# Kernel tuning notes

Measured on AMD Instinct MI355X. Metric: run time of the kernel, lower is better.

The kernel has to match this reference:

```python
import jax, jax.numpy as jnp
import numpy as np

B_IN, B_MID, B_OUT = 30, 16, 10   # band widths: input sphere, after S2 conv, after SO3 conv
F1, F2 = 100, 100                 # feature channels
EPS = 1e-5


def _qw(b):
    """Driscoll-Healy quadrature weights over the 2b beta samples (SOFT grid)."""
    j = np.arange(2 * b)
    k = np.arange(b)
    s = (np.sin(np.pi * (2 * j[:, None] + 1) * (2 * k[None, :] + 1) / (4 * b))
         / (2 * k[None, :] + 1)).sum(1)
    return ((2.0 / b) * np.sin(np.pi * (2 * j + 1) / (4 * b)) * s).astype(np.float32)


def _wigner_d_all(l_max, betas):
    """Wigner-d matrices d^l(beta) = exp(-i beta Jy) in the |l,m> basis (m = -l..l).
    Returns list over l of real arrays [n_beta, 2l+1, 2l+1]."""
    betas = np.asarray(betas, np.float64)
    out = []
    for l in range(l_max):
        m = np.arange(-l, l + 1)
        dim = 2 * l + 1
        Jp = np.zeros((dim, dim))
        for i in range(dim - 1):
            Jp[i + 1, i] = np.sqrt(l * (l + 1) - m[i] * (m[i] + 1))
        Jy = (Jp - Jp.T) / 2j
        ev, V = np.linalg.eigh(Jy)
        ph = np.exp(-1j * betas[:, None] * ev[None, :])
        d = np.einsum('ak,bk,ck->bac', V, ph, V.conj())
        out.append(np.real(d).astype(np.float32))
    return out


def _project(x, b):
    """Radial max-projection of a point cloud [B,3,N] onto a (beta,alpha) grid -> [B,1,2b,2b]."""
    r = jnp.sqrt(jnp.sum(x * x, axis=1) + 1e-12)                       # [B,N]
    beta = jnp.arccos(jnp.clip(x[:, 2] / r, -1 + 1e-7, 1 - 1e-7))      # [0,pi]
    alpha = jnp.mod(jnp.arctan2(x[:, 1], x[:, 0]), 2 * np.pi)          # [0,2pi)
    jb = jnp.clip((beta / np.pi * (2 * b)).astype(jnp.int32), 0, 2 * b - 1)
    ja = jnp.clip((alpha / (2 * np.pi) * (2 * b)).astype(jnp.int32), 0, 2 * b - 1)
    flat = jb * (2 * b) + ja
    img = jax.vmap(lambda f, v: jnp.zeros((2 * b) ** 2, x.dtype).at[f].max(v))(flat, r)
    return img.reshape(x.shape[0], 1, 2 * b, 2 * b)


def _s2_fft(x, dm0_w):
    """x: [B,F,2b,2b] (beta,alpha) -> list over l of x_hat [B,F,2l+1] (complex)."""
    X = jnp.fft.fft(x, axis=-1)     # FFT over alpha
    n = x.shape[-1]
    hats = []
    for l, dw in enumerate(dm0_w):
        idx = np.mod(np.arange(-l, l + 1), n)
        hats.append(jnp.einsum('pm,BFpm->BFm', jnp.asarray(dw), X[..., idx]))
    return hats


def _so3_fft(x, dmn_w):
    """x: [B,F,2b,2b,2b] (beta,alpha,gamma) -> list over l of [B,F,2l+1,2l+1]."""
    X = jnp.fft.fftn(x, axes=(-2, -1))   # FFT over alpha, gamma
    n = x.shape[-1]
    hats = []
    for l, dw in enumerate(dmn_w):
        idx = np.mod(np.arange(-l, l + 1), n)
        Xl = X[:, :, :, idx[:, None], idx[None, :]]        # [B,F,2b,2l+1,2l+1]
        hats.append(jnp.einsum('pmn,BFpmn->BFmn', jnp.asarray(dw), Xl))
    return hats


def _so3_ifft(hats, b, d_list):
    """list over l of [B,F,2l+1,2l+1] -> real SO(3) signal [B,F,2b,2b,2b]."""
    Bb, Ff = hats[0].shape[:2]
    n = 2 * b
    Fg = jnp.zeros((Bb, Ff, n, n, n), jnp.complex64)   # (beta, m, n) freq grid
    for l, h in enumerate(hats):
        idx = np.mod(np.arange(-l, l + 1), n)
        c = (2 * l + 1) * jnp.einsum('pmn,BFmn->BFpmn', jnp.asarray(d_list[l]), h)
        Fg = Fg.at[:, :, :, idx[:, None], idx[None, :]].add(c)
    return jnp.real(jnp.fft.ifft2(Fg, axes=(-2, -1)))


def _bn_relu(x, g, b):
    mu = jnp.mean(x, axis=(0, 2, 3, 4), keepdims=True)
    var = jnp.var(x, axis=(0, 2, 3, 4), keepdims=True)
    xn = (x - mu) * jax.lax.rsqrt(var + EPS)
    return jax.nn.relu(xn * g[None, :, None, None, None] + b[None, :, None, None, None])


def _forward(x, w_s2, b_s2, bn1_gamma, bn1_beta, w_so3, b_so3, bn2_gamma, bn2_beta):
    # constant tables (numpy, computed eagerly)
    betas_in = (np.arange(2 * B_IN) + 0.5) * np.pi / (2 * B_IN)
    betas_mid = (np.arange(2 * B_MID) + 0.5) * np.pi / (2 * B_MID)
    betas_out = (np.arange(2 * B_OUT) + 0.5) * np.pi / (2 * B_OUT)
    w_in, w_mid, w_out = _qw(B_IN), _qw(B_MID), _qw(B_OUT)
    d_in = _wigner_d_all(B_MID, betas_in)
    d_mid = _wigner_d_all(B_MID, betas_mid)
    d_out = _wigner_d_all(B_OUT, betas_out)
    d_eq = _wigner_d_all(B_MID, np.array([np.pi / 2]))   # equatorial grid beta = pi/2

    img = _project(x, B_IN)                              # [B,1,60,60]

    # ---- S2 convolution: band 30 -> 16 ----
    dm0_w = [d_in[l][:, :, l] * w_in[:, None] for l in range(B_MID)]   # d^l_{m0} * quad weights
    xhat = _s2_fft(img, dm0_w)                           # list of [B,1,2l+1]
    k_s2 = w_s2.shape[-1]
    a_s2 = 2 * np.pi * np.arange(k_s2) / k_s2
    ws = w_s2 * np.float32(1.0 / np.sqrt(k_s2 * 1 * B_MID ** 4 / B_IN ** 2))
    zhat = []
    for l in range(B_MID):
        m = np.arange(-l, l + 1)
        sh = (d_eq[l][0][:, l][None, :] * np.exp(-1j * np.outer(a_s2, m))).astype(np.complex64)  # [k,m]
        yh = jnp.einsum('km,iok->mio', jnp.asarray(sh), ws)           # kernel spectrum [2l+1,f_in,f_out]
        zhat.append(jnp.einsum('Bim,nio->Bomn', xhat[l], jnp.conj(yh)))  # outer product m x n
    z = _so3_ifft(zhat, B_MID, d_mid) + b_s2[None, :, None, None, None]  # [B,100,32,32,32]
    z = _bn_relu(z, bn1_gamma, bn1_beta)

    # ---- SO3 convolution: band 16 -> 10 ----
    dmn_w = [d_mid[l] * w_mid[:, None, None] for l in range(B_OUT)]
    xhat2 = _so3_fft(z, dmn_w)                           # list of [B,100,2l+1,2l+1]
    k_so3 = w_so3.shape[-1]
    a_so3 = 2 * np.pi * np.arange(k_so3) / k_so3
    wk = w_so3 * np.float32(1.0 / np.sqrt(k_so3 * F1 * B_OUT ** 3 / B_MID ** 3))
    zhat2 = []
    for l in range(B_OUT):
        m = np.arange(-l, l + 1)
        U = (d_eq[l][0][None] * np.exp(-1j * np.outer(a_so3, m))[:, :, None]).astype(np.complex64)  # [k,m,n], gamma=0
        yh = jnp.einsum('kmn,iok->mnio', jnp.asarray(U), wk)
        zhat2.append(jnp.einsum('Bimk,nkio->Bomn', xhat2[l], jnp.conj(yh)))  # z^l = x^l y^l+
    z2 = _so3_ifft(zhat2, B_OUT, d_out) + b_so3[None, :, None, None, None]   # [B,100,20,20,20]
    z2 = _bn_relu(z2, bn2_gamma, bn2_beta)

    # ---- so3_integrate: sum over alpha/gamma, quadrature-weighted sum over beta ----
    return jnp.einsum('BCpag,p->BC', z2, jnp.asarray(w_out))   # [B,100]


def setup_inputs() -> dict:
    key = jax.random.key(0)
    k0, k1, k2 = jax.random.split(key, 3)
    B, N = 8, 2048
    return {
        "x": jax.random.normal(k0, (B, 3, N), jnp.float32),
        "w_s2": jax.random.normal(k1, (1, F1, 2 * B_IN), jnp.float32),
        "b_s2": jnp.zeros((F1,), jnp.float32),
        "bn1_gamma": jnp.ones((F1,), jnp.float32),
        "bn1_beta": jnp.zeros((F1,), jnp.float32),
        "w_so3": jax.random.normal(k2, (F1, F2, 2 * B_MID), jnp.float32),
        "b_so3": jnp.zeros((F2,), jnp.float32),
        "bn2_gamma": jnp.ones((F2,), jnp.float32),
        "bn2_beta": jnp.zeros((F2,), jnp.float32),
    }


def reference(x, w_s2, b_s2, bn1_gamma, bn1_beta, w_so3, b_so3, bn2_gamma, bn2_beta):
    return _forward(x, w_s2, b_s2, bn1_gamma, bn1_beta, w_so3, b_so3, bn2_gamma, bn2_beta)
```

## Files before the change

### kernel.cpp

```cpp
#include <hip/hip_runtime.h>
#include <math.h>

#define PI_D 3.14159265358979323846

constexpr int NBATCH = 8;
constexpr int NPTS   = 2048;
constexpr int F1C    = 100;
constexpr int F2C    = 100;

__host__ __device__ constexpr int S2c(int l){ return l*(2*l-1)*(2*l+1)/3; }

constexpr int OFF_WIN   = 0;
constexpr int OFF_WMID  = OFF_WIN + 60;
constexpr int OFF_WOUTQ = OFF_WMID + 32;
constexpr int OFF_DM0W  = OFF_WOUTQ + 20;
constexpr int OFF_DMID  = OFF_DM0W + 60*256;
constexpr int OFF_DOUT  = OFF_DMID + 32*S2c(16);
constexpr int OFF_DEQ   = OFF_DOUT + 20*S2c(10);
constexpr int OFF_IMG   = OFF_DEQ + S2c(16);
constexpr int OFF_XF    = OFF_IMG + NBATCH*60*60;
constexpr int OFF_XHAT  = OFF_XF + NBATCH*60*31*2;
constexpr int OFF_WS2   = OFF_XHAT + NBATCH*256*2;
constexpr int OFF_BN1   = OFF_WS2 + 100*31*2;
constexpr int OFF_BN1AB = OFF_BN1 + 200;
constexpr int OFF_BN2   = OFF_BN1AB + 200;
constexpr int OFF_BN2AB = OFF_BN2 + 200;
constexpr int OFF_LUTA  = OFF_BN2AB + 200;
constexpr int OFF_LUTB  = OFF_LUTA + 1330;
constexpr int OFF_WCONV = OFF_LUTB + 1330;
constexpr int OFF_XHAT2 = OFF_WCONV + 100*100*19*2;
constexpr int OFF_SBUF  = OFF_XHAT2 + NBATCH*100*S2c(10)*2;
constexpr int OFF_ZHAT2 = OFF_SBUF + NBATCH*100*S2c(10)*2;
constexpr int OFF_Z2    = OFF_ZHAT2 + NBATCH*100*S2c(10)*2;
constexpr int OFF_Z     = OFF_Z2 + NBATCH*100*20*20*20;
constexpr int WS_TOTAL  = OFF_Z + NBATCH*100*32*32*32;
constexpr int OFF_HBUF  = OFF_Z2;

__device__ __forceinline__ int S2d(int l){ return l*(2*l-1)*(2*l+1)/3; }

__global__ void k_quad(float* ws){
  int j = threadIdx.x;
  if (j < 60){
    double bb = 30.0, s = 0.0;
    for (int k = 0; k < 30; ++k) s += sin(PI_D*(2*j+1)*(2*k+1)/(4.0*bb))/(2*k+1);
    ws[OFF_WIN+j] = (float)(2.0/bb * sin(PI_D*(2*j+1)/(4.0*bb)) * s);
  }
  if (j < 32){
    double bb = 16.0, s = 0.0;
    for (int k = 0; k < 16; ++k) s += sin(PI_D*(2*j+1)*(2*k+1)/(4.0*bb))/(2*k+1);
    ws[OFF_WMID+j] = (float)(2.0/bb * sin(PI_D*(2*j+1)/(4.0*bb)) * s);
  }
  if (j < 20){
    double bb = 10.0, s = 0.0;
    for (int k = 0; k < 10; ++k) s += sin(PI_D*(2*j+1)*(2*k+1)/(4.0*bb))/(2*k+1);
    ws[OFF_WOUTQ+j] = (float)(2.0/bb * sin(PI_D*(2*j+1)/(4.0*bb)) * s);
  }
}

__global__ void k_lut(float* ws){
  int q = blockIdx.x*blockDim.x + threadIdx.x;
  if (q >= 1330) return;
  int l = 0; while (S2d(l+1) <= q) ++l;
  int loc = q - S2d(l), tl = 2*l+1;
  int mm = loc/tl, nn = loc%tl;
  ((int*)(ws+OFF_LUTA))[q] = 32*S2d(l) + mm*tl + nn;
  ((int*)(ws+OFF_LUTB))[q] = ((mm-l+9)*19 + (nn-l+9)) | ((tl*tl) << 9) | ((nn-l+9) << 19);
}

__device__ double dev_wigner_t(const double* fact, int l, int mp, int m, double beta){
  double ch = cos(0.5*beta), sh = sin(0.5*beta);
  int kmin = m - mp; if (kmin < 0) kmin = 0;
  int kmax = l + m; if (l - mp < kmax) kmax = l - mp;
  double pref = sqrt(fact[l+mp]*fact[l-mp]*fact[l+m]*fact[l-m]);
  int ec = 2*l + m - mp - 2*kmin, es = mp - m + 2*kmin;
  double cp = 1.0, sp = 1.0;
  for (int e = 0; e < ec; ++e) cp *= ch;
  for (int e = 0; e < es; ++e) sp *= sh;
  double ch2i = 1.0/(ch*ch), sh2 = sh*sh;
  double sum = 0.0;
  for (int k = kmin; k <= kmax; ++k){
    double t = 1.0/(fact[l+m-k]*fact[k]*fact[l-mp-k]*fact[mp-m+k]);
    if ((mp-m+k) & 1) t = -t;
    sum += t*cp*sp;
    cp *= ch2i; sp *= sh2;
  }
  return pref*sum;
}

constexpr int N_DM0W = 60*256;
constexpr int N_DMID = 32*S2c(16);
constexpr int N_DOUT = 20*S2c(10);
constexpr int N_DEQ  = S2c(16);
constexpr int N_WIG  = N_DM0W + N_DMID + N_DOUT + N_DEQ;

__global__ void k_wigner(float* ws){
  __shared__ double fact[32];
  if (threadIdx.x == 0){ fact[0] = 1.0; for (int i = 1; i < 32; ++i) fact[i] = fact[i-1]*i; }
  __syncthreads();
  int idx = blockIdx.x*blockDim.x + threadIdx.x;
  if (idx >= N_WIG) return;
  if (idx < N_DM0W){
    int l = 0; while (60*(l+1)*(l+1) <= idx) ++l;
    int rem = idx - 60*l*l, tl = 2*l+1;
    int p = rem/tl, mm = rem%tl;
    double beta = (p+0.5)*PI_D/60.0;
    ws[OFF_DM0W+idx] = (float)dev_wigner_t(fact, l, mm-l, 0, beta) * ws[OFF_WIN+p];
    return;
  }
  idx -= N_DM0W;
  if (idx < N_DMID){
    int l = 0; while (32*S2d(l+1) <= idx) ++l;
    int rem = idx - 32*S2d(l), tl = 2*l+1;
    int q = rem % (tl*tl), p = rem/(tl*tl);
    int mm = q/tl, nn = q%tl;
    double beta = (p+0.5)*PI_D/32.0;
    ws[OFF_DMID+idx] = (float)dev_wigner_t(fact, l, mm-l, nn-l, beta);
    return;
  }
  idx -= N_DMID;
  if (idx < N_DOUT){
    int l = 0; while (20*S2d(l+1) <= idx) ++l;
    int rem = idx - 20*S2d(l), tl = 2*l+1;
    int q = rem % (tl*tl), p = rem/(tl*tl);
    int mm = q/tl, nn = q%tl;
    double beta = (p+0.5)*PI_D/20.0;
    ws[OFF_DOUT+idx] = (float)dev_wigner_t(fact, l, mm-l, nn-l, beta);
    return;
  }
  idx -= N_DOUT;
  {
    int l = 0; while (S2d(l+1) <= idx) ++l;
    int rem = idx - S2d(l), tl = 2*l+1;
    int mm = rem/tl, nn = rem%tl;
    ws[OFF_DEQ+idx] = (float)dev_wigner_t(fact, l, mm-l, nn-l, 0.5*PI_D);
  }
}

__global__ void k_project(const float* __restrict__ x, float* ws){
  int t = blockIdx.x*blockDim.x + threadIdx.x;
  if (t >= NBATCH*NPTS) return;
  int b = t / NPTS, n = t % NPTS;
  const float* xb = x + (size_t)b*3*NPTS;
  float xx = xb[n], yy = xb[NPTS+n], zz = xb[2*NPTS+n];
  float r = sqrtf(xx*xx + yy*yy + zz*zz + 1e-12f);
  float ct = zz / r;
  ct = fminf(fmaxf(ct, -1.0f + 1e-7f), 1.0f - 1e-7f);
  float beta = acosf(ct);
  float alpha = atan2f(yy, xx);
  if (alpha < 0.0f) alpha += 2.0f*(float)PI_D;
  int jb = (int)((beta / (float)PI_D) * 60.0f);
  jb = jb < 0 ? 0 : (jb > 59 ? 59 : jb);
  int ja = (int)((alpha / (2.0f*(float)PI_D)) * 60.0f);
  ja = ja < 0 ? 0 : (ja > 59 ? 59 : ja);
  unsigned* img = (unsigned*)(ws + OFF_IMG) + (b*3600 + jb*60 + ja);
  atomicMax(img, __float_as_uint(r));
}

__global__ void k_s2dft(float* ws){
  int t = blockIdx.x*blockDim.x + threadIdx.x;
  if (t >= NBATCH*60*31) return;
  int b = t/(60*31), r = t%(60*31);
  int p = r/31, mi = r%31, m = mi - 15;
  const float* img = ws + OFF_IMG + (b*60 + p)*60;
  float sr = 0.f, si = 0.f;
  for (int a = 0; a < 60; ++a){
    int k = ((a*m) % 60 + 60) % 60;
    float c = cospif(k/30.0f), s = sinpif(k/30.0f);
    float v = img[a];
    sr += v*c; si -= v*s;
  }
  ws[OFF_XF + t*2]   = sr;
  ws[OFF_XF + t*2+1] = si;
}

__global__ void k_xhat(float* ws){
  int t = blockIdx.x*blockDim.x + threadIdx.x;
  if (t >= NBATCH*256) return;
  int b = t/256, flat = t%256;
  int l = 0; while ((l+1)*(l+1) <= flat) ++l;
  int mm = flat - l*l, tl = 2*l+1;
  int mi = mm - l + 15;
  float sr = 0.f, si = 0.f;
  for (int p = 0; p < 60; ++p){
    float w = ws[OFF_DM0W + 60*l*l + p*tl + mm];
    sr += w * ws[OFF_XF + ((b*60+p)*31 + mi)*2];
    si += w * ws[OFF_XF + ((b*60+p)*31 + mi)*2 + 1];
  }
  ws[OFF_XHAT + t*2]   = sr;
  ws[OFF_XHAT + t*2+1] = si;
}

__global__ void k_ws2(float* ws, const float* __restrict__ w_s2, float scale1){
  int t = blockIdx.x*blockDim.x + threadIdx.x;
  if (t >= 100*31) return;
  int o = t/31, ni = t%31, n = ni - 15;
  float sr = 0.f, si = 0.f;
  for (int k = 0; k < 60; ++k){
    int kk = ((k*n) % 60 + 60) % 60;
    float c = cospif(kk/30.0f), s = sinpif(kk/30.0f);
    float v = w_s2[o*60 + k] * scale1;
    sr += v*c; si += v*s;
  }
  ws[OFF_WS2 + t*2]   = sr;
  ws[OFF_WS2 + t*2+1] = si;
}

__global__ __launch_bounds__(256) void k_H(float* ws){
  int bid = blockIdx.x;
  int p = bid & 31, b = bid >> 5;
  __shared__ float xh[512], Dt[256];
  __shared__ int dbase[16];
  int tid = threadIdx.x;
  {
    int flat = tid;
    int l = 0; while ((l+1)*(l+1) <= flat) ++l;
    int mm = flat - l*l, tl = 2*l+1;
    xh[2*flat]   = ws[OFF_XHAT + (b*256+flat)*2];
    xh[2*flat+1] = ws[OFF_XHAT + (b*256+flat)*2+1];
    Dt[flat] = (float)tl * ws[OFF_DEQ + S2d(l) + mm*tl + l];
  }
  if (tid < 16){ int l = tid, tl = 2*l+1; dbase[l] = OFF_DMID + 32*S2d(l) + p*tl*tl; }
  __syncthreads();
  float* Hb = ws + OFF_HBUF + (size_t)bid*992;
  for (int q = tid; q < 496; q += 256){
    int m = q/31, ni = q%31, n = ni-15;
    int an = n < 0 ? -n : n;
    int lmin = m > an ? m : an;
    float ar = 0.f, ai = 0.f;
    for (int l = lmin; l < 16; ++l){
      int tl = 2*l+1;
      float d = ws[dbase[l] + (m+l)*tl + (n+l)];
      float t = d * Dt[l*l + (n+l)];
      int fa = l*l + (m+l);
      ar += t*xh[2*fa]; ai += t*xh[2*fa+1];
    }
    Hb[2*q] = ar; Hb[2*q+1] = ai;
  }
}

__global__ __launch_bounds__(256) void k_so3ifft_mid(float* ws, const float* __restrict__ b_s2){
  int bid = blockIdx.x;
  int p = bid & 31, bo = bid >> 5;
  int o = bo % F1C, b = bo / F1C;
  __shared__ float Fg[992], tmpS[1024];
  __shared__ float twr[32], twi[32], Wr[31], Wi[31], redA[4], redB[4];
  int tid = threadIdx.x;
  if (tid < 32){ twr[tid] = cospif(tid/16.0f); twi[tid] = sinpif(tid/16.0f); }
  if (tid < 31){ Wr[tid] = ws[OFF_WS2 + (o*31+tid)*2]; Wi[tid] = ws[OFF_WS2 + (o*31+tid)*2+1]; }
  __syncthreads();
  {
    const float* Hb = ws + OFF_HBUF + (size_t)((b<<5)|p)*992;
    for (int q = tid; q < 496; q += 256){
      int ni = q % 31;
      float hr = Hb[2*q], hi = Hb[2*q+1];
      float wr = Wr[ni], wi = Wi[ni];
      Fg[2*q]   = hr*wr - hi*wi;
      Fg[2*q+1] = hr*wi + hi*wr;
    }
  }
  __syncthreads();
  if (tid < 128){
    int m = tid >> 3, g0 = tid & 7;
    float T0r=0,T0i=0,T1r=0,T1i=0,T2r=0,T2i=0,T3r=0,T3i=0;
    int base = 2*m*31;
    #pragma unroll
    for (int ni = 0; ni < 31; ++ni){
      int k = ((ni-15)*g0) & 31;
      float c = twr[k], s = twi[k];
      float fr = Fg[base+2*ni], fi = Fg[base+2*ni+1];
      float re = fr*c - fi*s, im = fr*s + fi*c;
      int cc = (ni+1) & 3;
      if (cc == 0){ T0r += re; T0i += im; }
      else if (cc == 1){ T1r += re; T1i += im; }
      else if (cc == 2){ T2r += re; T2i += im; }
      else { T3r += re; T3i += im; }
    }
    float Ar=T0r+T2r, Ai=T0i+T2i, Br=T0r-T2r, Bi=T0i-T2i;
    float Cr=T1r+T3r, Ci=T1i+T3i, Dr=T1r-T3r, Di=T1i-T3i;
    int ix = 2*(m*32+g0);
    tmpS[ix]      = Ar+Cr; tmpS[ix+1]    = Ai+Ci;
    tmpS[ix+16]   = Br-Di; tmpS[ix+17]   = Bi+Dr;
    tmpS[ix+32]   = Ar-Cr; tmpS[ix+33]   = Ai-Ci;
    tmpS[ix+48]   = Br+Di; tmpS[ix+49]   = Bi-Dr;
  }
  __syncthreads();
  float bsv = b_s2[o];
  float lsum = 0.f, lss = 0.f;
  float* z = ws + OFF_Z;
  size_t zb = ((size_t)(b*F1C+o)*32 + p)*1024;
  {
    int a0 = tid >> 5, g = tid & 31;
    float U0r=0, U2r=0, U1r=0, U1i=0, U3r=0, U3i=0;
    #pragma unroll
    for (int m = 1; m < 16; ++m){
      int k = (m*a0) & 31;
      float c = twr[k], s = twi[k];
      float tr = tmpS[2*(m*32+g)], ti = tmpS[2*(m*32+g)+1];
      float re = tr*c - ti*s;
      int cc = m & 3;
      if (cc == 0) U0r += re;
      else if (cc == 2) U2r += re;
      else {
        float im = tr*s + ti*c;
        if (cc == 1){ U1r += re; U1i += im; }
        else        { U3r += re; U3i += im; }
      }
    }
    float Ar = U0r + U2r, Br = U0r - U2r;
    float Cr = U1r + U3r, Di = U1i - U3i;
    float t0 = tmpS[2*g];
    float v0 = (t0 + 2.0f*(Ar + Cr))*(1.0f/1024.0f) + bsv;
    float v1 = (t0 + 2.0f*(Br - Di))*(1.0f/1024.0f) + bsv;
    float v2 = (t0 + 2.0f*(Ar - Cr))*(1.0f/1024.0f) + bsv;
    float v3 = (t0 + 2.0f*(Br + Di))*(1.0f/1024.0f) + bsv;
    z[zb + (a0     )*32 + g] = v0;
    z[zb + (a0 +  8)*32 + g] = v1;
    z[zb + (a0 + 16)*32 + g] = v2;
    z[zb + (a0 + 24)*32 + g] = v3;
    lsum = v0+v1+v2+v3;
    lss  = v0*v0+v1*v1+v2*v2+v3*v3;
  }
  for (int off = 32; off; off >>= 1){ lsum += __shfl_down(lsum, off); lss += __shfl_down(lss, off); }
  if ((tid & 63) == 0){ redA[tid>>6] = lsum; redB[tid>>6] = lss; }
  __syncthreads();
  if (tid == 0){
    atomicAdd(&ws[OFF_BN1 + o],       redA[0]+redA[1]+redA[2]+redA[3]);
    atomicAdd(&ws[OFF_BN1 + 100 + o], redB[0]+redB[1]+redB[2]+redB[3]);
  }
}

__global__ void k_bnfin1(float* ws, const float* __restrict__ g1, const float* __restrict__ be1){
  int t = threadIdx.x;
  if (t >= 100) return;
  const float invN = 1.0f/262144.0f;
  float mu = ws[OFF_BN1+t]*invN;
  float var = ws[OFF_BN1+100+t]*invN - mu*mu;
  float sA = rsqrtf(var + 1e-5f) * g1[t];
  ws[OFF_BN1AB+t]     = sA;
  ws[OFF_BN1AB+100+t] = be1[t] - mu*sA;
}

__global__ __launch_bounds__(256) void k_so3fft_a(float* ws){
  int bid = blockIdx.x;
  int p = bid & 31, bo = bid >> 5;
  int o = bo % F1C;
  __shared__ float y[32*33];
  __shared__ float Bs[32*36];
  __shared__ float t1[1216];
  __shared__ float twr[32], twi[32];
  int tid = threadIdx.x;
  if (tid < 32){ twr[tid] = cospif(tid/16.0f); twi[tid] = sinpif(tid/16.0f); }
  float sA = ws[OFF_BN1AB+o], sB = ws[OFF_BN1AB+100+o];
  float* zp = ws + OFF_Z + (size_t)bid*1024;
  for (int q = tid; q < 1024; q += 256){
    float v = zp[q]*sA + sB;
    y[(q>>5)*33 + (q&31)] = v > 0.f ? v : 0.f;
  }
  __syncthreads();
  {
    int a = tid >> 3, g2 = tid & 7;
    float y0 = y[a*33+g2], y1 = y[a*33+g2+8], y2 = y[a*33+g2+16], y3 = y[a*33+g2+24];
    float e = y0+y2, f = y1+y3;
    int bb = a*36 + g2*4;
    Bs[bb]   = e+f;
    Bs[bb+1] = e-f;
    Bs[bb+2] = y0-y2;
    Bs[bb+3] = -(y1-y3);
  }
  __syncthreads();
  for (int q = tid; q < 320; q += 256){
    int a = q/10, n = q%10, ni = 9+n;
    int c = n & 3;
    int bb = a*36;
    float sr = 0.f, si = 0.f;
    if ((c & 1) == 0){
      int off = bb + (c >> 1);
      #pragma unroll
      for (int g2 = 0; g2 < 8; ++g2){
        int k = (g2*n) & 31;
        float B = Bs[off + g2*4];
        sr += B*twr[k]; si -= B*twi[k];
      }
    } else {
      float sgn = (c == 1) ? 1.f : -1.f;
      #pragma unroll
      for (int g2 = 0; g2 < 8; ++g2){
        int k = (g2*n) & 31;
        float cc_ = twr[k], ss = twi[k];
        float br = Bs[bb+g2*4+2], bi = sgn*Bs[bb+g2*4+3];
        sr += br*cc_ + bi*ss;
        si += bi*cc_ - br*ss;
      }
    }
    t1[2*(a*19+ni)] = sr; t1[2*(a*19+ni)+1] = si;
  }
  __syncthreads();
  for (int q = tid; q < 160; q += 256){
    int a = q/10, ni = 9 + q%10;
    int i0 = 2*(a*19+ni), i1 = 2*((a+16)*19+ni);
    float xr=t1[i0], xi=t1[i0+1], yr=t1[i1], yi=t1[i1+1];
    t1[i0]=xr+yr; t1[i0+1]=xi+yi; t1[i1]=xr-yr; t1[i1+1]=xi-yi;
  }
  __syncthreads();
  float wm = ws[OFF_WMID+p];
  for (int q = tid; q < 190; q += 256){
    int m = q/10 - 9, nio = q%10, ni = 9+nio;
    int off = (m & 1) ? 16*19 : 0;
    float sr = 0.f, si = 0.f;
    for (int a = 0; a < 16; ++a){
      int k = (a*m) & 31;
      float c = twr[k], s = twi[k];
      float tr = t1[2*(off+a*19+ni)], ti = t1[2*(off+a*19+ni)+1];
      sr += tr*c + ti*s;
      si += ti*c - tr*s;
    }
    sr *= wm; si *= wm;
    int qf = (m+9)*19 + ni;
    zp[2*qf] = sr; zp[2*qf+1] = si;
    if (nio > 0){
      int qm = (9-m)*19 + (9-nio);
      zp[2*qm] = sr; zp[2*qm+1] = -si;
    }
  }
}

__global__ __launch_bounds__(512) void k_so3fft_b(float* ws){
  int bo = blockIdx.x;
  int tid = threadIdx.x;
  __shared__ float xw[722];
  const float* xwbase = ws + OFF_Z + (size_t)bo*32*1024;
  const int* lutA = (const int*)(ws + OFF_LUTA);
  const int* lutB = (const int*)(ws + OFF_LUTB);
  float accr[3], acci[3];
  int la[3], xi2[3], tl2v[3];
  #pragma unroll
  for (int j = 0; j < 3; ++j){
    accr[j] = 0.f; acci[j] = 0.f;
    int q = tid + 512*j;
    if (q < 1330){ la[j] = lutA[q]; int lb = lutB[q]; xi2[j] = 2*(lb & 511); tl2v[j] = (lb >> 9) & 1023; }
    else { la[j] = 0; xi2[j] = 0; tl2v[j] = 0; }
  }
  for (int pp = 0; pp < 32; ++pp){
    __syncthreads();
    for (int u = tid; u < 722; u += 512) xw[u] = xwbase[pp*1024 + u];
    __syncthreads();
    #pragma unroll
    for (int j = 0; j < 3; ++j){
      int q = tid + 512*j;
      if (q < 1330){
        float d = ws[OFF_DMID + la[j] + pp*tl2v[j]];
        accr[j] += d*xw[xi2[j]]; acci[j] += d*xw[xi2[j]+1];
      }
    }
  }
  #pragma unroll
  for (int j = 0; j < 3; ++j){
    int q = tid + 512*j;
    if (q < 1330){
      int base = OFF_XHAT2 + (bo*1330 + q)*2;
      ws[base]   = accr[j];
      ws[base+1] = acci[j];
    }
  }
}

__global__ void k_wconv(float* ws, const float* __restrict__ w_so3, float scale2){
  int t = blockIdx.x*blockDim.x + threadIdx.x;
  if (t >= 100*100*19) return;
  int ni = t % 19, io = t / 19;
  int n = ni - 9;
  float sr = 0.f, si = 0.f;
  for (int j = 0; j < 32; ++j){
    int k = (j*n) & 31;
    float c = cospif(k/16.0f), s = sinpif(k/16.0f);
    float v = w_so3[io*32 + j] * scale2;
    sr += v*c; si += v*s;
  }
  ws[OFF_WCONV + t*2]   = sr;
  ws[OFF_WCONV + t*2+1] = si;
}

__global__ void k_S(float* ws){
  int t = blockIdx.x*blockDim.x + threadIdx.x;
  if (t >= NBATCH*100*1330) return;
  int q = t % 1330, bi = t / 1330;
  int l = 0; while (S2d(l+1) <= q) ++l;
  int loc = q - S2d(l), tl = 2*l+1;
  int mm = loc/tl, nn = loc%tl;
  float sr = 0.f, si = 0.f;
  int xbase = OFF_XHAT2 + (bi*1330 + S2d(l) + mm*tl)*2;
  int dbase = OFF_DEQ + S2d(l) + nn*tl;
  for (int k = 0; k < tl; ++k){
    float d = ws[dbase + k];
    sr += d * ws[xbase + 2*k];
    si += d * ws[xbase + 2*k + 1];
  }
  ws[OFF_SBUF + t*2]   = sr;
  ws[OFF_SBUF + t*2+1] = si;
}

__global__ void k_zhat2(float* ws){
  int t = blockIdx.x*blockDim.x + threadIdx.x;
  if (t >= NBATCH*100*1330) return;
  int q = t % 1330, bo = t / 1330;
  int o = bo % 100, b = bo / 100;
  int lb = ((const int*)(ws+OFF_LUTB))[q];
  int ni = (lb >> 19) & 31;
  const float* sp = ws + OFF_SBUF + (size_t)(b*100)*2660 + 2*q;
  const float* wp = ws + OFF_WCONV + (size_t)(o*19 + ni)*2;
  float sr = 0.f, si = 0.f;
  for (int i = 0; i < 100; ++i){
    float Sr = sp[0], Si = sp[1];
    float Wr = wp[0], Wi = wp[1];
    sr += Sr*Wr - Si*Wi;
    si += Sr*Wi + Si*Wr;
    sp += 2660;
    wp += 3800;
  }
  ws[OFF_ZHAT2 + ((size_t)bo*1330 + q)*2]     = sr;
  ws[OFF_ZHAT2 + ((size_t)bo*1330 + q)*2 + 1] = si;
}

__global__ __launch_bounds__(256) void k_so3ifft_out(float* ws, const float* __restrict__ b_so3){
  int bid = blockIdx.x;
  int pg = bid % 5, bo = bid / 5;
  int o = bo % F2C, b = bo / F2C;
  __shared__ __align__(16) float zh[2660];
  __shared__ float Fg[380], tmpS[400];
  __shared__ float twr[20], twi[20], redA[4], redB[4];
  int tid = threadIdx.x;
  {
    const float4* zsrc = (const float4*)(ws + OFF_ZHAT2 + (size_t)bo*2660);
    float4* zds = (float4*)zh;
    for (int q = tid; q < 665; q += 256) zds[q] = zsrc[q];
  }
  if (tid < 20){ twr[tid] = cospif(tid/10.0f); twi[tid] = sinpif(tid/10.0f); }
  __syncthreads();
  float bsv = b_so3[o];
  float lsum = 0.f, lss = 0.f;
  float* z2 = ws + OFF_Z2;
  for (int pp = 0; pp < 4; ++pp){
    int p = pg*4 + pp;
    for (int q = tid; q < 190; q += 256){
      int m = q/19, ni = q%19, n = ni-9;
      int an = n < 0 ? -n : n;
      int lmin = m > an ? m : an;
      float ar = 0.f, ai = 0.f;
      for (int l = lmin; l < 10; ++l){
        int tl = 2*l+1;
        float d = ws[OFF_DOUT + 20*S2d(l) + (p*tl + (m+l))*tl + (n+l)] * (float)tl;
        int fz = S2d(l) + (m+l)*tl + (n+l);
        ar += d*zh[2*fz]; ai += d*zh[2*fz+1];
      }
      Fg[2*q] = ar; Fg[2*q+1] = ai;
    }
    __syncthreads();
    for (int q = tid; q < 100; q += 256){
      int m = q/10, g = q%10;
      float Er=0.f, Ei=0.f, Or=0.f, Oi=0.f;
      int base = 2*m*19;
      for (int ni = 1; ni < 19; ni += 2){
        int n = ni-9;
        int k = ((n*g) % 20 + 20) % 20;
        float c = twr[k], s = twi[k];
        float fr = Fg[base+2*ni], fi = Fg[base+2*ni+1];
        Er += fr*c - fi*s; Ei += fr*s + fi*c;
      }
      for (int ni = 0; ni < 19; ni += 2){
        int n = ni-9;
        int k = ((n*g) % 20 + 20) % 20;
        float c = twr[k], s = twi[k];
        float fr = Fg[base+2*ni], fi = Fg[base+2*ni+1];
        Or += fr*c - fi*s; Oi += fr*s + fi*c;
      }
      tmpS[2*(m*20+g)]      = Er+Or; tmpS[2*(m*20+g)+1]      = Ei+Oi;
      tmpS[2*(m*20+g+10)]   = Er-Or; tmpS[2*(m*20+g+10)+1]   = Ei-Oi;
    }
    __syncthreads();
    size_t zb = ((size_t)bo*20 + p)*400;
    for (int q = tid; q < 200; q += 256){
      int a = q/20, g = q%20;
      float E = 0.f, O = 0.f;
      for (int m = 2; m < 10; m += 2){
        int k = (m*a) % 20;
        E += tmpS[2*(m*20+g)]*twr[k] - tmpS[2*(m*20+g)+1]*twi[k];
      }
      for (int m = 1; m < 10; m += 2){
        int k = (m*a) % 20;
        O += tmpS[2*(m*20+g)]*twr[k] - tmpS[2*(m*20+g)+1]*twi[k];
      }
      float t0 = tmpS[2*g];
      float v1 = (t0 + 2.0f*(E+O))*(1.0f/400.0f) + bsv;
      float v2 = (t0 + 2.0f*(E-O))*(1.0f/400.0f) + bsv;
      z2[zb + a*20 + g]       = v1;
      z2[zb + (a+10)*20 + g]  = v2;
      lsum += v1+v2; lss += v1*v1+v2*v2;
    }
    __syncthreads();
  }
  for (int off = 32; off; off >>= 1){ lsum += __shfl_down(lsum, off); lss += __shfl_down(lss, off); }
  if ((tid & 63) == 0){ redA[tid>>6] = lsum; redB[tid>>6] = lss; }
  __syncthreads();
  if (tid == 0){
    atomicAdd(&ws[OFF_BN2 + o],       redA[0]+redA[1]+redA[2]+redA[3]);
    atomicAdd(&ws[OFF_BN2 + 100 + o], redB[0]+redB[1]+redB[2]+redB[3]);
  }
}

__global__ void k_bnfin2(float* ws, const float* __restrict__ g2, const float* __restrict__ be2){
  int t = threadIdx.x;
  if (t >= 100) return;
  const float invN = 1.0f/64000.0f;
  float mu = ws[OFF_BN2+t]*invN;
  float var = ws[OFF_BN2+100+t]*invN - mu*mu;
  float sA = rsqrtf(var + 1e-5f) * g2[t];
  ws[OFF_BN2AB+t]     = sA;
  ws[OFF_BN2AB+100+t] = be2[t] - mu*sA;
}

__global__ __launch_bounds__(256) void k_final(float* ws, float* __restrict__ out){
  int bid = blockIdx.x;
  int c = bid % 100, b = bid / 100;
  int tid = threadIdx.x;
  float sA = ws[OFF_BN2AB+c], sB = ws[OFF_BN2AB+100+c];
  const float* z2 = ws + OFF_Z2 + (size_t)(b*100+c)*8000;
  float lsum = 0.f;
  for (int q = tid; q < 8000; q += 256){
    int p = q / 400;
    float v = z2[q]*sA + sB;
    v = v > 0.f ? v : 0.f;
    lsum += v * ws[OFF_WOUTQ + p];
  }
  for (int off = 32; off; off >>= 1) lsum += __shfl_down(lsum, off);
  __shared__ float red[4];
  if ((tid & 63) == 0) red[tid>>6] = lsum;
  __syncthreads();
  if (tid == 0) out[b*100 + c] = red[0]+red[1]+red[2]+red[3];
}

extern "C" void kernel_launch(void* const* d_in, const int* in_sizes, int n_in,
                              void* d_out, int out_size, void* d_ws, size_t ws_size,
                              hipStream_t stream){
  const float* x      = (const float*)d_in[0];
  const float* w_s2   = (const float*)d_in[1];
  const float* b_s2   = (const float*)d_in[2];
  const float* g1     = (const float*)d_in[3];
  const float* be1    = (const float*)d_in[4];
  const float* w_so3  = (const float*)d_in[5];
  const float* b_so3  = (const float*)d_in[6];
  const float* g2     = (const float*)d_in[7];
  const float* be2    = (const float*)d_in[8];
  float* ws  = (float*)d_ws;
  float* out = (float*)d_out;

  hipMemsetAsync(ws + OFF_IMG, 0, NBATCH*3600*sizeof(float), stream);
  hipMemsetAsync(ws + OFF_BN1, 0, 200*sizeof(float), stream);
  hipMemsetAsync(ws + OFF_BN2, 0, 200*sizeof(float), stream);

  k_quad<<<1, 128, 0, stream>>>(ws);
  k_lut<<<6, 256, 0, stream>>>(ws);
  k_wigner<<<(N_WIG + 255)/256, 256, 0, stream>>>(ws);
  k_project<<<(NBATCH*NPTS + 255)/256, 256, 0, stream>>>(x, ws);
  k_s2dft<<<(NBATCH*60*31 + 255)/256, 256, 0, stream>>>(ws);
  k_xhat<<<(NBATCH*256 + 255)/256, 256, 0, stream>>>(ws);
  float scale1 = (float)(1.0/sqrt(60.0*1.0*65536.0/900.0));
  k_ws2<<<(100*31 + 255)/256, 256, 0, stream>>>(ws, w_s2, scale1);
  k_H<<<NBATCH*32, 256, 0, stream>>>(ws);
  k_so3ifft_mid<<<NBATCH*F1C*32, 256, 0, stream>>>(ws, b_s2);
  k_bnfin1<<<1, 128, 0, stream>>>(ws, g1, be1);
  k_so3fft_a<<<NBATCH*F1C*32, 256, 0, stream>>>(ws);
  k_so3fft_b<<<NBATCH*F1C, 512, 0, stream>>>(ws);
  float scale2 = (float)(1.0/sqrt(32.0*100.0*1000.0/4096.0));
  k_wconv<<<(100*100*19 + 255)/256, 256, 0, stream>>>(ws, w_so3, scale2);
  k_S<<<(NBATCH*100*1330 + 255)/256, 256, 0, stream>>>(ws);
  k_zhat2<<<(NBATCH*100*1330 + 255)/256, 256, 0, stream>>>(ws);
  k_so3ifft_out<<<NBATCH*F2C*5, 256, 0, stream>>>(ws, b_so3);
  k_bnfin2<<<1, 128, 0, stream>>>(ws, g2, be2);
  k_final<<<NBATCH*100, 256, 0, stream>>>(ws, out);
}
```

Before: 541.2 us.

## Fuse S contraction into so3fft_b and process two channels per so3ifft_mid block

```diff
diff --git a/kernel.cpp b/kernel.cpp
--- a/kernel.cpp
+++ b/kernel.cpp
@@ -27,7 +27,8 @@
 constexpr int OFF_BN2AB = OFF_BN2 + 200;
 constexpr int OFF_LUTA  = OFF_BN2AB + 200;
 constexpr int OFF_LUTB  = OFF_LUTA + 1330;
-constexpr int OFF_WCONV = OFF_LUTB + 1330;
+constexpr int OFF_LUTC  = OFF_LUTB + 1330;
+constexpr int OFF_WCONV = OFF_LUTC + 1330;
 constexpr int OFF_XHAT2 = OFF_WCONV + 100*100*19*2;
 constexpr int OFF_SBUF  = OFF_XHAT2 + NBATCH*100*S2c(10)*2;
 constexpr int OFF_ZHAT2 = OFF_SBUF + NBATCH*100*S2c(10)*2;
@@ -65,6 +66,7 @@
   int mm = loc/tl, nn = loc%tl;
   ((int*)(ws+OFF_LUTA))[q] = 32*S2d(l) + mm*tl + nn;
   ((int*)(ws+OFF_LUTB))[q] = ((mm-l+9)*19 + (nn-l+9)) | ((tl*tl) << 9) | ((nn-l+9) << 19);
+  ((int*)(ws+OFF_LUTC))[q] = (S2d(l) + mm*tl) | ((S2d(l) + nn*tl) << 11) | (tl << 22);
 }
 
 __device__ double dev_wigner_t(const double* fact, int l, int mp, int m, double beta){
@@ -240,29 +242,37 @@
 
 __global__ __launch_bounds__(256) void k_so3ifft_mid(float* ws, const float* __restrict__ b_s2){
   int bid = blockIdx.x;
-  int p = bid & 31, bo = bid >> 5;
-  int o = bo % F1C, b = bo / F1C;
-  __shared__ float Fg[992], tmpS[1024];
-  __shared__ float twr[32], twi[32], Wr[31], Wi[31], redA[4], redB[4];
+  int p = bid & 31, boo = bid >> 5;
+  int oo = boo % 50, b = boo / 50;
+  int o0 = oo*2;
+  __shared__ float Fg[1984], tmpS[2048];
+  __shared__ float twr[32], twi[32], Wr[62], Wi[62], redA[8], redB[8];
   int tid = threadIdx.x;
   if (tid < 32){ twr[tid] = cospif(tid/16.0f); twi[tid] = sinpif(tid/16.0f); }
-  if (tid < 31){ Wr[tid] = ws[OFF_WS2 + (o*31+tid)*2]; Wi[tid] = ws[OFF_WS2 + (o*31+tid)*2+1]; }
+  if (tid < 62){
+    int oh = tid/31, ni = tid%31;
+    Wr[tid] = ws[OFF_WS2 + ((o0+oh)*31+ni)*2];
+    Wi[tid] = ws[OFF_WS2 + ((o0+oh)*31+ni)*2+1];
+  }
   __syncthreads();
   {
     const float* Hb = ws + OFF_HBUF + (size_t)((b<<5)|p)*992;
-    for (int q = tid; q < 496; q += 256){
-      int ni = q % 31;
-      float hr = Hb[2*q], hi = Hb[2*q+1];
-      float wr = Wr[ni], wi = Wi[ni];
+    for (int q = tid; q < 992; q += 256){
+      int half = q >= 496 ? 1 : 0;
+      int qq = q - half*496;
+      int ni = qq % 31;
+      float hr = Hb[2*qq], hi = Hb[2*qq+1];
+      float wr = Wr[half*31+ni], wi = Wi[half*31+ni];
       Fg[2*q]   = hr*wr - hi*wi;
       Fg[2*q+1] = hr*wi + hi*wr;
     }
   }
   __syncthreads();
-  if (tid < 128){
-    int m = tid >> 3, g0 = tid & 7;
+  {
+    int half = tid >> 7, w = tid & 127;
+    int m = w >> 3, g0 = w & 7;
     float T0r=0,T0i=0,T1r=0,T1i=0,T2r=0,T2i=0,T3r=0,T3i=0;
-    int base = 2*m*31;
+    int base = 2*(half*496 + m*31);
     #pragma unroll
     for (int ni = 0; ni < 31; ++ni){
       int k = ((ni-15)*g0) & 31;
@@ -277,55 +287,67 @@
     }
     float Ar=T0r+T2r, Ai=T0i+T2i, Br=T0r-T2r, Bi=T0i-T2i;
     float Cr=T1r+T3r, Ci=T1i+T3i, Dr=T1r-T3r, Di=T1i-T3i;
-    int ix = 2*(m*32+g0);
+    int ix = 2*(half*512 + m*32 + g0);
     tmpS[ix]      = Ar+Cr; tmpS[ix+1]    = Ai+Ci;
     tmpS[ix+16]   = Br-Di; tmpS[ix+17]   = Bi+Dr;
     tmpS[ix+32]   = Ar-Cr; tmpS[ix+33]   = Ai-Ci;
     tmpS[ix+48]   = Br+Di; tmpS[ix+49]   = Bi-Dr;
   }
   __syncthreads();
-  float bsv = b_s2[o];
-  float lsum = 0.f, lss = 0.f;
+  float lsumA[2] = {0.f, 0.f}, lssA[2] = {0.f, 0.f};
   float* z = ws + OFF_Z;
-  size_t zb = ((size_t)(b*F1C+o)*32 + p)*1024;
   {
     int a0 = tid >> 5, g = tid & 31;
-    float U0r=0, U2r=0, U1r=0, U1i=0, U3r=0, U3i=0;
-    #pragma unroll
-    for (int m = 1; m < 16; ++m){
-      int k = (m*a0) & 31;
-      float c = twr[k], s = twi[k];
-      float tr = tmpS[2*(m*32+g)], ti = tmpS[2*(m*32+g)+1];
-      float re = tr*c - ti*s;
-      int cc = m & 3;
-      if (cc == 0) U0r += re;
-      else if (cc == 2) U2r += re;
-      else {
-        float im = tr*s + ti*c;
-        if (cc == 1){ U1r += re; U1i += im; }
-        else        { U3r += re; U3i += im; }
-      }
-    }
-    float Ar = U0r + U2r, Br = U0r - U2r;
-    float Cr = U1r + U3r, Di = U1i - U3i;
-    float t0 = tmpS[2*g];
-    float v0 = (t0 + 2.0f*(Ar + Cr))*(1.0f/1024.0f) + bsv;
-    float v1 = (t0 + 2.0f*(Br - Di))*(1.0f/1024.0f) + bsv;
-    float v2 = (t0 + 2.0f*(Ar - Cr))*(1.0f/1024.0f) + bsv;
-    float v3 = (t0 + 2.0f*(Br + Di))*(1.0f/1024.0f) + bsv;
-    z[zb + (a0     )*32 + g] = v0;
-    z[zb + (a0 +  8)*32 + g] = v1;
-    z[zb + (a0 + 16)*32 + g] = v2;
-    z[zb + (a0 + 24)*32 + g] = v3;
-    lsum = v0+v1+v2+v3;
-    lss  = v0*v0+v1*v1+v2*v2+v3*v3;
-  }
-  for (int off = 32; off; off >>= 1){ lsum += __shfl_down(lsum, off); lss += __shfl_down(lss, off); }
-  if ((tid & 63) == 0){ redA[tid>>6] = lsum; redB[tid>>6] = lss; }
+    for (int half = 0; half < 2; ++half){
+      float bsv = b_s2[o0+half];
+      int tb = half*512;
+      float U0r=0, U2r=0, U1r=0, U1i=0, U3r=0, U3i=0;
+      #pragma unroll
+      for (int m = 1; m < 16; ++m){
+        int k = (m*a0) & 31;
+        float c = twr[k], s = twi[k];
+        float tr = tmpS[2*(tb + m*32+g)], ti = tmpS[2*(tb + m*32+g)+1];
+        float re = tr*c - ti*s;
+        int cc = m & 3;
+        if (cc == 0) U0r += re;
+        else if (cc == 2) U2r += re;
+        else {
+          float im = tr*s + ti*c;
+          if (cc == 1){ U1r += re; U1i += im; }
+          else        { U3r += re; U3i += im; }
+        }
+      }
+      float Ar = U0r + U2r, Br = U0r - U2r;
+      float Cr = U1r + U3r, Di = U1i - U3i;
+      float t0 = tmpS[2*(tb + g)];
+      float v0 = (t0 + 2.0f*(Ar + Cr))*(1.0f/1024.0f) + bsv;
+      float v1 = (t0 + 2.0f*(Br - Di))*(1.0f/1024.0f) + bsv;
+      float v2 = (t0 + 2.0f*(Ar - Cr))*(1.0f/1024.0f) + bsv;
+      float v3 = (t0 + 2.0f*(Br + Di))*(1.0f/1024.0f) + bsv;
+      size_t zb = ((size_t)(b*F1C + o0+half)*32 + p)*1024;
+      z[zb + (a0     )*32 + g] = v0;
+      z[zb + (a0 +  8)*32 + g] = v1;
+      z[zb + (a0 + 16)*32 + g] = v2;
+      z[zb + (a0 + 24)*32 + g] = v3;
+      lsumA[half] = v0+v1+v2+v3;
+      lssA[half]  = v0*v0+v1*v1+v2*v2+v3*v3;
+    }
+  }
+  for (int off = 32; off; off >>= 1){
+    lsumA[0] += __shfl_down(lsumA[0], off); lssA[0] += __shfl_down(lssA[0], off);
+    lsumA[1] += __shfl_down(lsumA[1], off); lssA[1] += __shfl_down(lssA[1], off);
+  }
+  if ((tid & 63) == 0){
+    int wv = tid >> 6;
+    redA[wv]   = lsumA[0]; redB[wv]   = lssA[0];
+    redA[4+wv] = lsumA[1]; redB[4+wv] = lssA[1];
+  }
   __syncthreads();
   if (tid == 0){
-    atomicAdd(&ws[OFF_BN1 + o],       redA[0]+redA[1]+redA[2]+redA[3]);
-    atomicAdd(&ws[OFF_BN1 + 100 + o], redB[0]+redB[1]+redB[2]+redB[3]);
+    atomicAdd(&ws[OFF_BN1 + o0],       redA[0]+redA[1]+redA[2]+redA[3]);
+    atomicAdd(&ws[OFF_BN1 + 100 + o0], redB[0]+redB[1]+redB[2]+redB[3]);
+    atomicAdd(&ws[OFF_BN1 + o0+1],       redA[4]+redA[5]+redA[6]+redA[7]);
+    atomicAdd(&ws[OFF_BN1 + 100 + o0+1], redB[4]+redB[5]+redB[6]+redB[7]);
   }
 }
 
@@ -428,9 +450,11 @@
   int bo = blockIdx.x;
   int tid = threadIdx.x;
   __shared__ float xw[722];
+  __shared__ float xh2[2660];
   const float* xwbase = ws + OFF_Z + (size_t)bo*32*1024;
   const int* lutA = (const int*)(ws + OFF_LUTA);
   const int* lutB = (const int*)(ws + OFF_LUTB);
+  const int* lutC = (const int*)(ws + OFF_LUTC);
   float accr[3], acci[3];
   int la[3], xi2[3], tl2v[3];
   #pragma unroll
@@ -456,10 +480,25 @@
   #pragma unroll
   for (int j = 0; j < 3; ++j){
     int q = tid + 512*j;
+    if (q < 1330){ xh2[2*q] = accr[j]; xh2[2*q+1] = acci[j]; }
+  }
+  __syncthreads();
+  #pragma unroll
+  for (int j = 0; j < 3; ++j){
+    int q = tid + 512*j;
     if (q < 1330){
-      int base = OFF_XHAT2 + (bo*1330 + q)*2;
-      ws[base]   = accr[j];
-      ws[base+1] = acci[j];
+      int lc = lutC[q];
+      int rowstart = lc & 2047, deqrow = (lc >> 11) & 2047, tl = lc >> 22;
+      const float* dq = ws + OFF_DEQ + deqrow;
+      const float* xb = xh2 + 2*rowstart;
+      float sr = 0.f, si = 0.f;
+      for (int k = 0; k < tl; ++k){
+        float d = dq[k];
+        sr += d*xb[2*k]; si += d*xb[2*k+1];
+      }
+      int base = OFF_SBUF + (bo*1330 + q)*2;
+      ws[base]   = sr;
+      ws[base+1] = si;
     }
   }
 }
@@ -478,25 +517,6 @@
   }
   ws[OFF_WCONV + t*2]   = sr;
   ws[OFF_WCONV + t*2+1] = si;
-}
-
-__global__ void k_S(float* ws){
-  int t = blockIdx.x*blockDim.x + threadIdx.x;
-  if (t >= NBATCH*100*1330) return;
-  int q = t % 1330, bi = t / 1330;
-  int l = 0; while (S2d(l+1) <= q) ++l;
-  int loc = q - S2d(l), tl = 2*l+1;
-  int mm = loc/tl, nn = loc%tl;
-  float sr = 0.f, si = 0.f;
-  int xbase = OFF_XHAT2 + (bi*1330 + S2d(l) + mm*tl)*2;
-  int dbase = OFF_DEQ + S2d(l) + nn*tl;
-  for (int k = 0; k < tl; ++k){
-    float d = ws[dbase + k];
-    sr += d * ws[xbase + 2*k];
-    si += d * ws[xbase + 2*k + 1];
-  }
-  ws[OFF_SBUF + t*2]   = sr;
-  ws[OFF_SBUF + t*2+1] = si;
 }
 
 __global__ void k_zhat2(float* ws){
@@ -666,13 +686,12 @@
   float scale1 = (float)(1.0/sqrt(60.0*1.0*65536.0/900.0));
   k_ws2<<<(100*31 + 255)/256, 256, 0, stream>>>(ws, w_s2, scale1);
   k_H<<<NBATCH*32, 256, 0, stream>>>(ws);
-  k_so3ifft_mid<<<NBATCH*F1C*32, 256, 0, stream>>>(ws, b_s2);
+  k_so3ifft_mid<<<NBATCH*50*32, 256, 0, stream>>>(ws, b_s2);
   k_bnfin1<<<1, 128, 0, stream>>>(ws, g1, be1);
   k_so3fft_a<<<NBATCH*F1C*32, 256, 0, stream>>>(ws);
   k_so3fft_b<<<NBATCH*F1C, 512, 0, stream>>>(ws);
   float scale2 = (float)(1.0/sqrt(32.0*100.0*1000.0/4096.0));
   k_wconv<<<(100*100*19 + 255)/256, 256, 0, stream>>>(ws, w_so3, scale2);
-  k_S<<<(NBATCH*100*1330 + 255)/256, 256, 0, stream>>>(ws);
   k_zhat2<<<(NBATCH*100*1330 + 255)/256, 256, 0, stream>>>(ws);
   k_so3ifft_out<<<NBATCH*F2C*5, 256, 0, stream>>>(ws, b_so3);
   k_bnfin2<<<1, 128, 0, stream>>>(ws, g2, be2);
```

Measured after the change: 515.0 us. -4.8%, faster.

## Fuse S-transform into SO3 FFT kernel and register-block zhat2 over output pairs

Applied to the files above, without the earlier changes.

```diff
diff --git a/kernel.cpp b/kernel.cpp
--- a/kernel.cpp
+++ b/kernel.cpp
@@ -27,7 +27,8 @@
 constexpr int OFF_BN2AB = OFF_BN2 + 200;
 constexpr int OFF_LUTA  = OFF_BN2AB + 200;
 constexpr int OFF_LUTB  = OFF_LUTA + 1330;
-constexpr int OFF_WCONV = OFF_LUTB + 1330;
+constexpr int OFF_LUTC  = OFF_LUTB + 1330;
+constexpr int OFF_WCONV = OFF_LUTC + 1330;
 constexpr int OFF_XHAT2 = OFF_WCONV + 100*100*19*2;
 constexpr int OFF_SBUF  = OFF_XHAT2 + NBATCH*100*S2c(10)*2;
 constexpr int OFF_ZHAT2 = OFF_SBUF + NBATCH*100*S2c(10)*2;
@@ -65,6 +66,7 @@
   int mm = loc/tl, nn = loc%tl;
   ((int*)(ws+OFF_LUTA))[q] = 32*S2d(l) + mm*tl + nn;
   ((int*)(ws+OFF_LUTB))[q] = ((mm-l+9)*19 + (nn-l+9)) | ((tl*tl) << 9) | ((nn-l+9) << 19);
+  ((int*)(ws+OFF_LUTC))[q] = (S2d(l) + mm*tl) | ((S2d(l) + nn*tl) << 11) | (tl << 22);
 }
 
 __device__ double dev_wigner_t(const double* fact, int l, int mp, int m, double beta){
@@ -428,9 +430,11 @@
   int bo = blockIdx.x;
   int tid = threadIdx.x;
   __shared__ float xw[722];
+  __shared__ float xh2[2660];
   const float* xwbase = ws + OFF_Z + (size_t)bo*32*1024;
   const int* lutA = (const int*)(ws + OFF_LUTA);
   const int* lutB = (const int*)(ws + OFF_LUTB);
+  const int* lutC = (const int*)(ws + OFF_LUTC);
   float accr[3], acci[3];
   int la[3], xi2[3], tl2v[3];
   #pragma unroll
@@ -456,10 +460,25 @@
   #pragma unroll
   for (int j = 0; j < 3; ++j){
     int q = tid + 512*j;
+    if (q < 1330){ xh2[2*q] = accr[j]; xh2[2*q+1] = acci[j]; }
+  }
+  __syncthreads();
+  #pragma unroll
+  for (int j = 0; j < 3; ++j){
+    int q = tid + 512*j;
     if (q < 1330){
-      int base = OFF_XHAT2 + (bo*1330 + q)*2;
-      ws[base]   = accr[j];
-      ws[base+1] = acci[j];
+      int lc = lutC[q];
+      int rowstart = lc & 2047, deqrow = (lc >> 11) & 2047, tl = lc >> 22;
+      const float* dq = ws + OFF_DEQ + deqrow;
+      const float* xb = xh2 + 2*rowstart;
+      float sr = 0.f, si = 0.f;
+      for (int k = 0; k < tl; ++k){
+        float d = dq[k];
+        sr += d*xb[2*k]; si += d*xb[2*k+1];
+      }
+      int base = OFF_SBUF + (bo*1330 + q)*2;
+      ws[base]   = sr;
+      ws[base+1] = si;
     }
   }
 }
@@ -480,45 +499,35 @@
   ws[OFF_WCONV + t*2+1] = si;
 }
 
-__global__ void k_S(float* ws){
-  int t = blockIdx.x*blockDim.x + threadIdx.x;
-  if (t >= NBATCH*100*1330) return;
-  int q = t % 1330, bi = t / 1330;
-  int l = 0; while (S2d(l+1) <= q) ++l;
-  int loc = q - S2d(l), tl = 2*l+1;
-  int mm = loc/tl, nn = loc%tl;
-  float sr = 0.f, si = 0.f;
-  int xbase = OFF_XHAT2 + (bi*1330 + S2d(l) + mm*tl)*2;
-  int dbase = OFF_DEQ + S2d(l) + nn*tl;
-  for (int k = 0; k < tl; ++k){
-    float d = ws[dbase + k];
-    sr += d * ws[xbase + 2*k];
-    si += d * ws[xbase + 2*k + 1];
-  }
-  ws[OFF_SBUF + t*2]   = sr;
-  ws[OFF_SBUF + t*2+1] = si;
-}
-
 __global__ void k_zhat2(float* ws){
   int t = blockIdx.x*blockDim.x + threadIdx.x;
-  if (t >= NBATCH*100*1330) return;
-  int q = t % 1330, bo = t / 1330;
-  int o = bo % 100, b = bo / 100;
+  if (t >= NBATCH*50*1330) return;
+  int q = t % 1330, boo = t / 1330;
+  int oq = boo % 50, b = boo / 50;
+  int o0 = oq*2;
   int lb = ((const int*)(ws+OFF_LUTB))[q];
   int ni = (lb >> 19) & 31;
-  const float* sp = ws + OFF_SBUF + (size_t)(b*100)*2660 + 2*q;
-  const float* wp = ws + OFF_WCONV + (size_t)(o*19 + ni)*2;
-  float sr = 0.f, si = 0.f;
+  const float* sp  = ws + OFF_SBUF + (size_t)(b*100)*2660 + 2*q;
+  const float* wp0 = ws + OFF_WCONV + (size_t)(o0*19 + ni)*2;
+  const float* wp1 = wp0 + 38;
+  float sr0 = 0.f, si0 = 0.f, sr1 = 0.f, si1 = 0.f;
   for (int i = 0; i < 100; ++i){
     float Sr = sp[0], Si = sp[1];
-    float Wr = wp[0], Wi = wp[1];
-    sr += Sr*Wr - Si*Wi;
-    si += Sr*Wi + Si*Wr;
+    float W0r = wp0[0], W0i = wp0[1];
+    float W1r = wp1[0], W1i = wp1[1];
+    sr0 += Sr*W0r - Si*W0i;
+    si0 += Sr*W0i + Si*W0r;
+    sr1 += Sr*W1r - Si*W1i;
+    si1 += Sr*W1i + Si*W1r;
     sp += 2660;
-    wp += 3800;
-  }
-  ws[OFF_ZHAT2 + ((size_t)bo*1330 + q)*2]     = sr;
-  ws[OFF_ZHAT2 + ((size_t)bo*1330 + q)*2 + 1] = si;
+    wp0 += 3800;
+    wp1 += 3800;
+  }
+  size_t zb0 = ((size_t)(b*100 + o0)*1330 + q)*2;
+  ws[OFF_ZHAT2 + zb0]          = sr0;
+  ws[OFF_ZHAT2 + zb0 + 1]      = si0;
+  ws[OFF_ZHAT2 + zb0 + 2660]   = sr1;
+  ws[OFF_ZHAT2 + zb0 + 2661]   = si1;
 }
 
 __global__ __launch_bounds__(256) void k_so3ifft_out(float* ws, const float* __restrict__ b_so3){
@@ -672,8 +681,7 @@
   k_so3fft_b<<<NBATCH*F1C, 512, 0, stream>>>(ws);
   float scale2 = (float)(1.0/sqrt(32.0*100.0*1000.0/4096.0));
   k_wconv<<<(100*100*19 + 255)/256, 256, 0, stream>>>(ws, w_so3, scale2);
-  k_S<<<(NBATCH*100*1330 + 255)/256, 256, 0, stream>>>(ws);
-  k_zhat2<<<(NBATCH*100*1330 + 255)/256, 256, 0, stream>>>(ws);
+  k_zhat2<<<(NBATCH*50*1330 + 255)/256, 256, 0, stream>>>(ws);
   k_so3ifft_out<<<NBATCH*F2C*5, 256, 0, stream>>>(ws, b_so3);
   k_bnfin2<<<1, 128, 0, stream>>>(ws, g2, be2);
   k_final<<<NBATCH*100, 256, 0, stream>>>(ws, out);
```

Result: faster. 498.0 us (-8.0%).
